# Kernel optimization log

Hardware: AMD Instinct MI355X
Metric: run time of the kernel (lower is better)

Reference implementation:

```python
import jax, jax.numpy as jnp
import numpy as np

B, L, D, S = 64, 1024, 1024, 32  # batch, tokens, feat dim, num attribute ids (labels 1..S; 0 = ignore)
EPS = 1e-8  # torch F.cosine_similarity eps


def setup_inputs() -> dict:
    key = jax.random.key(0)
    k1, k2, k3 = jax.random.split(key, 3)
    attributes = jax.random.randint(k1, (B, L), 0, S + 1, dtype=jnp.int32)
    # guarantee every label 1..S appears in each sample (so every segment mean is defined
    # and max(attribute) == S, matching the fixed-S vectorization of the original loop)
    attributes = attributes.at[:, :S].set(jnp.arange(1, S + 1, dtype=jnp.int32)[None, :])
    text_feats = jax.random.normal(k2, (B, L, D), dtype=jnp.float32)
    Vgs = jax.random.normal(k3, (B, S, D), dtype=jnp.float32)
    return {"attributes": attributes, "text_feats": text_feats, "Vgs": Vgs}


def reference(attributes, text_feats, Vgs):
    # one-hot over labels 1..S: [B, L, S]
    onehot = (attributes[..., None] == jnp.arange(1, S + 1, dtype=attributes.dtype)).astype(text_feats.dtype)
    # segment sums and counts -> per-attribute mean feature: [B, S, D]
    seg_sum = jnp.einsum('bls,bld->bsd', onehot, text_feats)
    seg_cnt = jnp.sum(onehot, axis=1)  # [B, S]
    seg_mean = seg_sum / seg_cnt[..., None]
    # cosine similarity per (sample, attribute), torch semantics with eps clamp
    num = jnp.sum(Vgs * seg_mean, axis=-1)  # [B, S]
    denom = jnp.maximum(jnp.linalg.norm(Vgs, axis=-1) * jnp.linalg.norm(seg_mean, axis=-1), EPS)
    cos = num / denom
    # per-sample: 1 - mean_over_attributes(cos); loss: mean over batch (count == B here)
    loss = jnp.mean(1.0 - jnp.mean(cos, axis=-1))
    return loss
```

## Files before the change

kernel.cpp:

```cpp
#include <hip/hip_runtime.h>

constexpr int Bx = 64;
constexpr int Lx = 1024;
constexpr int Dx = 1024;
constexpr int Sx = 32;

constexpr int LQ    = 256;
constexpr int NQ    = Lx / LQ;
constexpr int NSCAT = Bx * NQ;
constexpr int PREF  = 8;

__global__ __launch_bounds__(1024) void hist_kernel(
    const int* __restrict__ attrs, int* __restrict__ wcnt)
{
    __shared__ int hist[Sx + 1];
    const int b = blockIdx.x, tid = threadIdx.x;
    if (tid <= Sx) hist[tid] = 0;
    __syncthreads();
    atomicAdd(&hist[attrs[b * Lx + tid]], 1);
    __syncthreads();
    if (tid >= 1 && tid <= Sx) wcnt[b * Sx + (tid - 1)] = hist[tid];
}

__global__ __launch_bounds__(256, 1) void seg_scatter_kernel(
    const float* __restrict__ text,
    const int*   __restrict__ attrs,
    float* __restrict__ pseg)
{
    __shared__ int attrs_lds[LQ];

    const int tid = threadIdx.x;
    const int bid = blockIdx.x;
    const int b   = bid >> 2;
    const int q   = bid & 3;
    const int l0  = q * LQ;
    const int col = tid * 4;

    if (tid < LQ) attrs_lds[tid] = attrs[b * Lx + l0 + tid];
    __syncthreads();

    const float* __restrict__ tp =
        text + ((size_t)b * Lx + l0) * Dx + col;

    float4 acc[Sx];
    #pragma unroll
    for (int s = 0; s < Sx; ++s) acc[s] = make_float4(0.f, 0.f, 0.f, 0.f);

    float4 buf[PREF];
    #pragma unroll
    for (int j = 0; j < PREF; ++j)
        buf[j] = *(const float4*)(tp + (size_t)j * Dx);

#define ACC_CASE(K) case K:                                   \
        acc[K-1].x += v.x; acc[K-1].y += v.y;                 \
        acc[K-1].z += v.z; acc[K-1].w += v.w; break;

    for (int i0 = 0; i0 < LQ; i0 += PREF) {
        #pragma unroll
        for (int j = 0; j < PREF; ++j) {
            const float4 v = buf[j];
            const int    i = i0 + j;
            if (i + PREF < LQ)
                buf[j] = *(const float4*)(tp + (size_t)(i + PREF) * Dx);
            const int sa = __builtin_amdgcn_readfirstlane(attrs_lds[i]);
            switch (sa) {
                ACC_CASE(1)  ACC_CASE(2)  ACC_CASE(3)  ACC_CASE(4)
                ACC_CASE(5)  ACC_CASE(6)  ACC_CASE(7)  ACC_CASE(8)
                ACC_CASE(9)  ACC_CASE(10) ACC_CASE(11) ACC_CASE(12)
                ACC_CASE(13) ACC_CASE(14) ACC_CASE(15) ACC_CASE(16)
                ACC_CASE(17) ACC_CASE(18) ACC_CASE(19) ACC_CASE(20)
                ACC_CASE(21) ACC_CASE(22) ACC_CASE(23) ACC_CASE(24)
                ACC_CASE(25) ACC_CASE(26) ACC_CASE(27) ACC_CASE(28)
                ACC_CASE(29) ACC_CASE(30) ACC_CASE(31) ACC_CASE(32)
                default: break;
            }
        }
    }
#undef ACC_CASE

    float* __restrict__ op = pseg + (size_t)bid * Sx * Dx + col;
    #pragma unroll
    for (int s = 0; s < Sx; ++s)
        *(float4*)(op + (size_t)s * Dx) = acc[s];
}

__global__ __launch_bounds__(256) void reduce_kernel(
    const float* __restrict__ pseg,
    const float* __restrict__ vgs,
    float* __restrict__ pnum,
    float* __restrict__ pns2,
    float* __restrict__ pnv2)
{
    const int tid = threadIdx.x;
    const int bid = blockIdx.x;
    const int b   = bid >> 5;
    const int s   = bid & 31;
    const int col = tid * 4;

    float4 seg = make_float4(0.f, 0.f, 0.f, 0.f);
    #pragma unroll
    for (int q = 0; q < NQ; ++q) {
        const float4 p = *(const float4*)(
            pseg + ((size_t)((b * NQ + q) * Sx + s)) * Dx + col);
        seg.x += p.x; seg.y += p.y; seg.z += p.z; seg.w += p.w;
    }
    const float4 vv = *(const float4*)(vgs + (size_t)bid * Dx + col);

    float pn = seg.x * vv.x + seg.y * vv.y + seg.z * vv.z + seg.w * vv.w;
    float ps = seg.x * seg.x + seg.y * seg.y + seg.z * seg.z + seg.w * seg.w;
    float pv = vv.x * vv.x + vv.y * vv.y + vv.z * vv.z + vv.w * vv.w;

    #pragma unroll
    for (int off = 32; off > 0; off >>= 1) {
        pn += __shfl_xor(pn, off, 64);
        ps += __shfl_xor(ps, off, 64);
        pv += __shfl_xor(pv, off, 64);
    }
    __shared__ float red[3][4];
    if ((tid & 63) == 0) {
        red[0][tid >> 6] = pn; red[1][tid >> 6] = ps; red[2][tid >> 6] = pv;
    }
    __syncthreads();
    if (tid == 0) {
        pnum[bid] = red[0][0] + red[0][1] + red[0][2] + red[0][3];
        pns2[bid] = red[1][0] + red[1][1] + red[1][2] + red[1][3];
        pnv2[bid] = red[2][0] + red[2][1] + red[2][2] + red[2][3];
    }
}

__global__ __launch_bounds__(256) void finalize_kernel(
    const float* __restrict__ pnum, const float* __restrict__ pns2,
    const float* __restrict__ pnv2, const int* __restrict__ wcnt,
    float* __restrict__ out)
{
    const int tid = threadIdx.x;
    float lsum = 0.0f;
    #pragma unroll
    for (int k = 0; k < (Bx * Sx) / 256; ++k) {
        const int p = k * 256 + tid;
        const float cnt   = (float)wcnt[p];
        const float denom = fmaxf(sqrtf(pnv2[p]) * sqrtf(pns2[p]),
                                  1e-8f * cnt);
        lsum += pnum[p] / denom;
    }
    #pragma unroll
    for (int off = 32; off > 0; off >>= 1) lsum += __shfl_xor(lsum, off, 64);

    __shared__ float red[4];
    if ((tid & 63) == 0) red[tid >> 6] = lsum;
    __syncthreads();
    if (tid == 0) {
        const float total = red[0] + red[1] + red[2] + red[3];
        out[0] = 1.0f - total * (1.0f / (float)(Bx * Sx));
    }
}

extern "C" void kernel_launch(void* const* d_in, const int* in_sizes, int n_in,
                              void* d_out, int out_size, void* d_ws, size_t ws_size,
                              hipStream_t stream) {
    const int*   attrs = (const int*)d_in[0];
    const float* text  = (const float*)d_in[1];
    const float* vgs   = (const float*)d_in[2];
    float* out = (float*)d_out;

    float* pseg = (float*)d_ws;
    float* pnum = pseg + (size_t)NSCAT * Sx * Dx;
    float* pns2 = pnum + Bx * Sx;
    float* pnv2 = pns2 + Bx * Sx;
    int*   wcnt = (int*)(pnv2 + Bx * Sx);

    hist_kernel<<<Bx, 1024, 0, stream>>>(attrs, wcnt);
    seg_scatter_kernel<<<NSCAT, 256, 0, stream>>>(text, attrs, pseg);
    reduce_kernel<<<Bx * Sx, 256, 0, stream>>>(pseg, vgs, pnum, pns2, pnv2);
    finalize_kernel<<<1, 256, 0, stream>>>(pnum, pns2, pnv2, wcnt, out);
}
```

Measured before the change: 397.0 us.

## Accumulate segment sums with LDS atomics and fold counts into reduce kernel

The scatter kernel now keeps its 32 per-attribute accumulators in per-wave shared memory, updated with LDS atomicAdd, instead of a 128-register array driven by a switch. It also reads labels from registers via readlane and uses nontemporal loads and stores. The histogram kernel is removed: per-label counts and the cosine division move into the reduce kernel, and the finalize kernel becomes a plain sum, saving one launch. The trade is a large LDS footprint that keeps one block per CU, plus LDS atomic latency on every row in place of cheap register adds.

```diff
diff --git a/kernel.cpp b/kernel.cpp
--- a/kernel.cpp
+++ b/kernel.cpp
@@ -8,18 +8,17 @@
 constexpr int LQ    = 256;
 constexpr int NQ    = Lx / LQ;
 constexpr int NSCAT = Bx * NQ;
-constexpr int PREF  = 8;
+constexpr int PREF  = 4;
+constexpr int ROWS  = Sx + 1;
 
-__global__ __launch_bounds__(1024) void hist_kernel(
-    const int* __restrict__ attrs, int* __restrict__ wcnt)
-{
-    __shared__ int hist[Sx + 1];
-    const int b = blockIdx.x, tid = threadIdx.x;
-    if (tid <= Sx) hist[tid] = 0;
-    __syncthreads();
-    atomicAdd(&hist[attrs[b * Lx + tid]], 1);
-    __syncthreads();
-    if (tid >= 1 && tid <= Sx) wcnt[b * Sx + (tid - 1)] = hist[tid];
+typedef float  f32x4v __attribute__((ext_vector_type(4)));
+typedef int    i32x4v __attribute__((ext_vector_type(4)));
+
+__device__ __forceinline__ f32x4v nt_load4(const float* p) {
+    return __builtin_nontemporal_load((const f32x4v*)p);
+}
+__device__ __forceinline__ void nt_store4(float* p, f32x4v v) {
+    __builtin_nontemporal_store(v, (f32x4v*)p);
 }
 
 __global__ __launch_bounds__(256, 1) void seg_scatter_kernel(
@@ -27,84 +26,96 @@
     const int*   __restrict__ attrs,
     float* __restrict__ pseg)
 {
-    __shared__ int attrs_lds[LQ];
+    __shared__ float acc[4 * ROWS * 4 * 64];
 
-    const int tid = threadIdx.x;
-    const int bid = blockIdx.x;
-    const int b   = bid >> 2;
-    const int q   = bid & 3;
-    const int l0  = q * LQ;
-    const int col = tid * 4;
+    const int tid  = threadIdx.x;
+    const int bid  = blockIdx.x;
+    const int b    = bid & 63;
+    const int q    = bid >> 6;
+    const int l0   = q * LQ;
+    const int w    = tid >> 6;
+    const int lane = tid & 63;
 
-    if (tid < LQ) attrs_lds[tid] = attrs[b * Lx + l0 + tid];
-    __syncthreads();
+    float* __restrict__ accw = acc + w * (ROWS * 256);
+    {
+        f32x4v* az = (f32x4v*)accw;
+        #pragma unroll
+        for (int i = 0; i < (ROWS * 256) / 1024; ++i)
+            az[i * 256 + (lane * 4) / 4] = (f32x4v){0.f, 0.f, 0.f, 0.f};
+        #pragma unroll
+        for (int i = 0; i < 33; ++i)
+            az[i * 64 + lane] = (f32x4v){0.f, 0.f, 0.f, 0.f};
+    }
+
+    int attrs_v[4];
+    #pragma unroll
+    for (int k = 0; k < 4; ++k)
+        attrs_v[k] = attrs[b * Lx + l0 + k * 64 + lane];
 
     const float* __restrict__ tp =
-        text + ((size_t)b * Lx + l0) * Dx + col;
+        text + ((size_t)b * Lx + l0) * Dx + w * 256 + lane * 4;
 
-    float4 acc[Sx];
-    #pragma unroll
-    for (int s = 0; s < Sx; ++s) acc[s] = make_float4(0.f, 0.f, 0.f, 0.f);
-
-    float4 buf[PREF];
+    f32x4v buf[PREF];
     #pragma unroll
     for (int j = 0; j < PREF; ++j)
-        buf[j] = *(const float4*)(tp + (size_t)j * Dx);
+        buf[j] = nt_load4(tp + (size_t)j * Dx);
 
-#define ACC_CASE(K) case K:                                   \
-        acc[K-1].x += v.x; acc[K-1].y += v.y;                 \
-        acc[K-1].z += v.z; acc[K-1].w += v.w; break;
-
-    for (int i0 = 0; i0 < LQ; i0 += PREF) {
-        #pragma unroll
-        for (int j = 0; j < PREF; ++j) {
-            const float4 v = buf[j];
-            const int    i = i0 + j;
-            if (i + PREF < LQ)
-                buf[j] = *(const float4*)(tp + (size_t)(i + PREF) * Dx);
-            const int sa = __builtin_amdgcn_readfirstlane(attrs_lds[i]);
-            switch (sa) {
-                ACC_CASE(1)  ACC_CASE(2)  ACC_CASE(3)  ACC_CASE(4)
-                ACC_CASE(5)  ACC_CASE(6)  ACC_CASE(7)  ACC_CASE(8)
-                ACC_CASE(9)  ACC_CASE(10) ACC_CASE(11) ACC_CASE(12)
-                ACC_CASE(13) ACC_CASE(14) ACC_CASE(15) ACC_CASE(16)
-                ACC_CASE(17) ACC_CASE(18) ACC_CASE(19) ACC_CASE(20)
-                ACC_CASE(21) ACC_CASE(22) ACC_CASE(23) ACC_CASE(24)
-                ACC_CASE(25) ACC_CASE(26) ACC_CASE(27) ACC_CASE(28)
-                ACC_CASE(29) ACC_CASE(30) ACC_CASE(31) ACC_CASE(32)
-                default: break;
+    #pragma unroll
+    for (int k = 0; k < 4; ++k) {
+        for (int j0 = 0; j0 < 16; ++j0) {
+            #pragma unroll
+            for (int jj = 0; jj < PREF; ++jj) {
+                const int    i = k * 64 + j0 * PREF + jj;
+                const f32x4v v = buf[jj];
+                if (i + PREF < LQ)
+                    buf[jj] = nt_load4(tp + (size_t)(i + PREF) * Dx);
+                const int sa =
+                    __builtin_amdgcn_readlane(attrs_v[k], j0 * PREF + jj);
+                float* ap = accw + sa * 256 + lane;
+                atomicAdd(ap + 0 * 64, v.x);
+                atomicAdd(ap + 1 * 64, v.y);
+                atomicAdd(ap + 2 * 64, v.z);
+                atomicAdd(ap + 3 * 64, v.w);
             }
         }
     }
-#undef ACC_CASE
+    __syncthreads();
 
-    float* __restrict__ op = pseg + (size_t)bid * Sx * Dx + col;
+    float* __restrict__ op = pseg + (size_t)bid * Sx * Dx + tid * 4;
     #pragma unroll
-    for (int s = 0; s < Sx; ++s)
-        *(float4*)(op + (size_t)s * Dx) = acc[s];
+    for (int s = 0; s < Sx; ++s) {
+        const float* ap = accw + (s + 1) * 256 + lane;
+        f32x4v o;
+        o.x = ap[0 * 64]; o.y = ap[1 * 64];
+        o.z = ap[2 * 64]; o.w = ap[3 * 64];
+        nt_store4(op + (size_t)s * Dx, o);
+    }
 }
 
 __global__ __launch_bounds__(256) void reduce_kernel(
     const float* __restrict__ pseg,
     const float* __restrict__ vgs,
-    float* __restrict__ pnum,
-    float* __restrict__ pns2,
-    float* __restrict__ pnv2)
+    const int*   __restrict__ attrs,
+    float* __restrict__ cosg)
 {
     const int tid = threadIdx.x;
     const int bid = blockIdx.x;
-    const int b   = bid >> 5;
-    const int s   = bid & 31;
+    const int s   = bid >> 6;
+    const int b   = bid & 63;
     const int col = tid * 4;
 
-    float4 seg = make_float4(0.f, 0.f, 0.f, 0.f);
+    f32x4v seg = {0.f, 0.f, 0.f, 0.f};
     #pragma unroll
     for (int q = 0; q < NQ; ++q) {
-        const float4 p = *(const float4*)(
-            pseg + ((size_t)((b * NQ + q) * Sx + s)) * Dx + col);
-        seg.x += p.x; seg.y += p.y; seg.z += p.z; seg.w += p.w;
+        const f32x4v p = nt_load4(
+            pseg + ((size_t)(q * 64 + b) * Sx + s) * Dx + col);
+        seg += p;
     }
-    const float4 vv = *(const float4*)(vgs + (size_t)bid * Dx + col);
+    const f32x4v vv = nt_load4(vgs + ((size_t)b * Sx + s) * Dx + col);
+
+    const i32x4v a4 = *(const i32x4v*)(attrs + b * Lx + tid * 4);
+    float pc = (float)((a4.x == s + 1) + (a4.y == s + 1) +
+                       (a4.z == s + 1) + (a4.w == s + 1));
 
     float pn = seg.x * vv.x + seg.y * vv.y + seg.z * vv.z + seg.w * vv.w;
     float ps = seg.x * seg.x + seg.y * seg.y + seg.z * seg.z + seg.w * seg.w;
@@ -115,34 +126,32 @@
         pn += __shfl_xor(pn, off, 64);
         ps += __shfl_xor(ps, off, 64);
         pv += __shfl_xor(pv, off, 64);
+        pc += __shfl_xor(pc, off, 64);
     }
-    __shared__ float red[3][4];
+    __shared__ float red[4][4];
     if ((tid & 63) == 0) {
-        red[0][tid >> 6] = pn; red[1][tid >> 6] = ps; red[2][tid >> 6] = pv;
+        red[0][tid >> 6] = pn; red[1][tid >> 6] = ps;
+        red[2][tid >> 6] = pv; red[3][tid >> 6] = pc;
     }
     __syncthreads();
     if (tid == 0) {
-        pnum[bid] = red[0][0] + red[0][1] + red[0][2] + red[0][3];
-        pns2[bid] = red[1][0] + red[1][1] + red[1][2] + red[1][3];
-        pnv2[bid] = red[2][0] + red[2][1] + red[2][2] + red[2][3];
+        const float num = red[0][0] + red[0][1] + red[0][2] + red[0][3];
+        const float ns2 = red[1][0] + red[1][1] + red[1][2] + red[1][3];
+        const float nv2 = red[2][0] + red[2][1] + red[2][2] + red[2][3];
+        const float cnt = red[3][0] + red[3][1] + red[3][2] + red[3][3];
+        const float denom = fmaxf(sqrtf(nv2) * sqrtf(ns2), 1e-8f * cnt);
+        cosg[bid] = num / denom;
     }
 }
 
-__global__ __launch_bounds__(256) void finalize_kernel(
-    const float* __restrict__ pnum, const float* __restrict__ pns2,
-    const float* __restrict__ pnv2, const int* __restrict__ wcnt,
-    float* __restrict__ out)
+__global__ __launch_bounds__(256) void sum_kernel(
+    const float* __restrict__ cosg, float* __restrict__ out)
 {
     const int tid = threadIdx.x;
     float lsum = 0.0f;
     #pragma unroll
-    for (int k = 0; k < (Bx * Sx) / 256; ++k) {
-        const int p = k * 256 + tid;
-        const float cnt   = (float)wcnt[p];
-        const float denom = fmaxf(sqrtf(pnv2[p]) * sqrtf(pns2[p]),
-                                  1e-8f * cnt);
-        lsum += pnum[p] / denom;
-    }
+    for (int k = 0; k < (Bx * Sx) / 256; ++k)
+        lsum += cosg[k * 256 + tid];
     #pragma unroll
     for (int off = 32; off > 0; off >>= 1) lsum += __shfl_xor(lsum, off, 64);
 
@@ -164,13 +173,9 @@
     float* out = (float*)d_out;
 
     float* pseg = (float*)d_ws;
-    float* pnum = pseg + (size_t)NSCAT * Sx * Dx;
-    float* pns2 = pnum + Bx * Sx;
-    float* pnv2 = pns2 + Bx * Sx;
-    int*   wcnt = (int*)(pnv2 + Bx * Sx);
+    float* cosg = pseg + (size_t)NSCAT * Sx * Dx;
 
-    hist_kernel<<<Bx, 1024, 0, stream>>>(attrs, wcnt);
     seg_scatter_kernel<<<NSCAT, 256, 0, stream>>>(text, attrs, pseg);
-    reduce_kernel<<<Bx * Sx, 256, 0, stream>>>(pseg, vgs, pnum, pns2, pnv2);
-    finalize_kernel<<<1, 256, 0, stream>>>(pnum, pns2, pnv2, wcnt, out);
+    reduce_kernel<<<Bx * Sx, 256, 0, stream>>>(pseg, vgs, attrs, cosg);
+    sum_kernel<<<1, 256, 0, stream>>>(cosg, out);
 }
```

New measurement: 640.8 us. +61.4%, slower.
